# Kernel optimization log

Hardware: AMD Instinct MI355X
Metric: run time of the kernel (lower is better)

Reference implementation:

```python
import jax, jax.numpy as jnp
import numpy as np

EPS = 1e-12
W_MAX = 0.8
ALPHA_MAX = 1.5
EXP_CLIP = 20.0
UNARY_TEMP = 1.5
T = 10
ETA = 0.2
ALPHA_SCALE = 1.0

N_NODES = 50000
N_PAIRS = 400000          # undirected pairs; E = 2*N_PAIRS directed edges
IN_DIM = 256
HID = 128
C = 10
EDGE_HID = 64


def setup_inputs() -> dict:
    key = jax.random.key(0)
    ks = jax.random.split(key, 12)
    x = jax.random.normal(ks[0], (N_NODES, IN_DIM), dtype=jnp.float32)
    # symmetric edge list: each undirected pair appears in both directions,
    # rev[e] gives the index of the reversed edge
    src = jax.random.randint(ks[1], (N_PAIRS,), 0, N_NODES, dtype=jnp.int32)
    dst = jax.random.randint(ks[2], (N_PAIRS,), 0, N_NODES, dtype=jnp.int32)
    edge_index = jnp.stack([jnp.concatenate([src, dst]),
                            jnp.concatenate([dst, src])])  # [2, E]
    rev = jnp.concatenate([jnp.arange(N_PAIRS, 2 * N_PAIRS, dtype=jnp.int32),
                           jnp.arange(0, N_PAIRS, dtype=jnp.int32)])
    def lin(k, fan_in, fan_out):
        s = 1.0 / np.sqrt(fan_in)
        return jax.random.uniform(k, (fan_in, fan_out), jnp.float32, -s, s)
    enc_w1 = lin(ks[3], IN_DIM, HID); enc_b1 = jnp.zeros((HID,), jnp.float32)
    enc_w2 = lin(ks[4], HID, C);      enc_b2 = jnp.zeros((C,), jnp.float32)
    em_in = 2 * HID + 2
    em_w1 = lin(ks[5], em_in, EDGE_HID); em_b1 = jnp.zeros((EDGE_HID,), jnp.float32)
    em_w2 = lin(ks[6], EDGE_HID, 1);     em_b2 = jnp.zeros((1,), jnp.float32)
    # xavier_uniform for R_raw
    bound = np.sqrt(6.0 / (C + C))
    R_raw = jax.random.uniform(ks[7], (C, C), jnp.float32, -bound, bound)
    R_scale_log = jnp.asarray(0.0, jnp.float32)
    msg_logit = jnp.asarray(-1.0, jnp.float32)
    return {"x": x, "edge_index": edge_index, "rev": rev,
            "enc_w1": enc_w1, "enc_b1": enc_b1, "enc_w2": enc_w2, "enc_b2": enc_b2,
            "em_w1": em_w1, "em_b1": em_b1, "em_w2": em_w2, "em_b2": em_b2,
            "R_raw": R_raw, "R_scale_log": R_scale_log, "msg_logit": msg_logit}


def reference(x, edge_index, rev, enc_w1, enc_b1, enc_w2, enc_b2,
              em_w1, em_b1, em_w2, em_b2, R_raw, R_scale_log, msg_logit):
    num_nodes = x.shape[0]
    src, dst = edge_index[0], edge_index[1]

    # --- UnaryEncoder (mlp, eval mode: no dropout) ---
    h = jax.nn.relu(x @ enc_w1 + enc_b1)                       # [N, H]
    logits = h @ enc_w2 + enc_b2                               # [N, C]
    log_phi = jax.nn.log_softmax(logits / UNARY_TEMP, axis=-1)

    # --- edge structural features ---
    deg = jax.ops.segment_sum(jnp.ones_like(src, jnp.float32), src,
                              num_segments=num_nodes)           # bincount(src)
    logdeg = jnp.log(deg + 1.0)
    a, b = logdeg[src], logdeg[dst]
    struct = jnp.stack([a + b, jnp.abs(a - b)], axis=-1)        # [E, 2]

    # --- pairwise kernel ---
    hs, hd = h[src], h[dst]
    edge_in = jnp.concatenate([hs * hd, jnp.abs(hs - hd), struct], axis=-1)
    w_raw = (jax.nn.relu(edge_in @ em_w1 + em_b1) @ em_w2 + em_b2)[:, 0]
    w = W_MAX * jax.nn.sigmoid(w_raw)
    w = 0.5 * (w + w[rev])                                      # symmetrize
    R = (jax.nn.softplus(R_scale_log) + 1e-6) * jnp.tanh(0.5 * (R_raw + R_raw.T))
    K = jnp.exp(jnp.clip(w[:, None, None] * R[None], -EXP_CLIP, EXP_CLIP))  # [E,C,C]

    # --- BP ---
    deg_c = jnp.maximum(deg, 1.0)
    edge_norm = (deg_c[src] * deg_c[dst]) ** -0.5               # [E]
    alpha = ALPHA_MAX * jax.nn.sigmoid(msg_logit) * ALPHA_SCALE
    lp_src = log_phi[src]
    m0 = jax.nn.softmax(lp_src, axis=-1)                        # init_unary=True

    def step(m, _):
        f = jnp.einsum('ec,ecd->ed', m, K)
        f = jnp.nan_to_num(f, nan=1.0, posinf=1.0, neginf=1.0)
        log_f = jnp.log(jnp.maximum(f, EPS)) * edge_norm[:, None]
        sum_in = jax.ops.segment_sum(log_f, dst, num_segments=num_nodes)
        excl = sum_in[src] - log_f[rev]
        m_new = jax.nn.softmax(lp_src + alpha * excl, axis=-1)
        m = (1.0 - ETA) * m + ETA * m_new
        m = jnp.maximum(m, EPS)
        m = m / jnp.sum(m, axis=-1, keepdims=True)
        return m, None

    m, _ = jax.lax.scan(step, m0, None, length=T)

    # --- beliefs ---
    f = jnp.einsum('ec,ecd->ed', m, K)
    f = jnp.nan_to_num(f, nan=1.0, posinf=1.0, neginf=1.0)
    log_f = jnp.log(jnp.maximum(f, EPS)) * edge_norm[:, None]
    sum_in = jax.ops.segment_sum(log_f, dst, num_segments=num_nodes)
    beliefs = jax.nn.softmax(log_phi + alpha * sum_in, axis=-1)  # [N, C]
    return beliefs
```

## Files before the change

kernel.cpp:

```cpp
#include <hip/hip_runtime.h>
#include <hip/hip_fp16.h>

#define NN 50000
#define NP 400000
#define NEDGE 800000
#define IND 256
#define HD 128
#define NC 10
#define TBP 10
#define SCAN_NB 196

typedef _Float16 f16;
typedef _Float16 f16x2 __attribute__((ext_vector_type(2)));
typedef _Float16 f16x4 __attribute__((ext_vector_type(4)));
typedef _Float16 f16x8 __attribute__((ext_vector_type(8)));
typedef unsigned short u16x8 __attribute__((ext_vector_type(8)));
typedef float f32x4 __attribute__((ext_vector_type(4)));

static constexpr size_t OFF_R      = 0;
static constexpr size_t OFF_H      = 512;
static constexpr size_t OFF_OFFS   = 512;
static constexpr size_t OFF_CUR    = 512 + 200016;
static constexpr size_t OFF_CSR    = 512 + 400032;
static constexpr size_t OFF_BSUM   = 512 + 3600032;
static constexpr size_t OFF_BBASE  = 512 + 3601056;
static constexpr size_t OFF_LOGPHI = 12800512;
static constexpr size_t OFF_DEG    = 14800512;
static constexpr size_t OFF_LOGDEG = 15000512;
static constexpr size_t OFF_RSQ    = 15200512;
static constexpr size_t OFF_WPAIR  = 15400512;
static constexpr size_t OFF_EN     = 17000512;
static constexpr size_t OFF_M      = 18600512;
static constexpr size_t OFF_L      = 50600512;
static constexpr size_t OFF_SUMIN  = 82600512;
static constexpr size_t OFF_W1T    = 84600512;
static constexpr size_t OFF_W1TE   = 84633280;

__global__ __launch_bounds__(256) void k_setup(const float* __restrict__ Rraw,
    const float* __restrict__ rsl, const float* __restrict__ ml,
    const float* __restrict__ mw1, const float* __restrict__ ew1,
    float* __restrict__ Rbuf, f16* __restrict__ w1t, f16* __restrict__ w1te) {
  int tid = threadIdx.x;
  if (tid < 100) {
    int c = tid / 10, d = tid % 10;
    float scale = log1pf(expf(rsl[0])) + 1e-6f;
    Rbuf[tid] = scale * tanhf(0.5f * (Rraw[c * 10 + d] + Rraw[d * 10 + c]));
  } else if (tid == 100) {
    Rbuf[100] = 1.5f * (1.f / (1.f + expf(-ml[0])));
  }
  for (int idx = tid; idx < 64 * 256; idx += 256) {
    int j = idx >> 8, k = idx & 255;
    w1t[idx] = (f16)mw1[k * 64 + j];
  }
  for (int idx = tid; idx < 128 * 256; idx += 256) {
    int j = idx >> 8, k = idx & 255;
    w1te[idx] = (f16)ew1[k * HD + j];
  }
}

__global__ __launch_bounds__(256) void k_deg(const int* __restrict__ ei, float* __restrict__ deg) {
  int e = blockIdx.x * 256 + threadIdx.x;
  if (e < NEDGE) atomicAdd(&deg[ei[e]], 1.f);
}

__global__ __launch_bounds__(256) void k_nodepost(const float* __restrict__ deg,
    float* __restrict__ logdeg, float* __restrict__ rsq) {
  int i = blockIdx.x * 256 + threadIdx.x;
  if (i >= NN) return;
  float d = deg[i];
  logdeg[i] = __logf(d + 1.f);
  rsq[i] = rsqrtf(fmaxf(d, 1.f));
}

__global__ __launch_bounds__(256) void k_scan1(const float* __restrict__ deg,
    int* __restrict__ bsum) {
  int idx = blockIdx.x * 256 + threadIdx.x;
  int v = (idx < NN) ? (int)deg[idx] : 0;
#pragma unroll
  for (int o = 32; o; o >>= 1) v += __shfl_down(v, o);
  __shared__ int wsum[4];
  if ((threadIdx.x & 63) == 0) wsum[threadIdx.x >> 6] = v;
  __syncthreads();
  if (threadIdx.x == 0) bsum[blockIdx.x] = wsum[0] + wsum[1] + wsum[2] + wsum[3];
}

__global__ __launch_bounds__(256) void k_scan2(const int* __restrict__ bsum,
    int* __restrict__ bbase) {
  __shared__ int s[256];
  int t = threadIdx.x;
  int orig = (t < SCAN_NB) ? bsum[t] : 0;
  s[t] = orig;
  __syncthreads();
  for (int d = 1; d < 256; d <<= 1) {
    int v = (t >= d) ? s[t - d] : 0;
    __syncthreads();
    s[t] += v;
    __syncthreads();
  }
  bbase[t] = s[t] - orig;
}

__global__ __launch_bounds__(256) void k_scan3(const float* __restrict__ deg,
    const int* __restrict__ bbase, int* __restrict__ off, int* __restrict__ cursor) {
  __shared__ int s[256];
  int t = threadIdx.x;
  int idx = blockIdx.x * 256 + t;
  int d = (idx < NN) ? (int)deg[idx] : 0;
  s[t] = d;
  __syncthreads();
  for (int k = 1; k < 256; k <<= 1) {
    int v = (t >= k) ? s[t - k] : 0;
    __syncthreads();
    s[t] += v;
    __syncthreads();
  }
  int base = bbase[blockIdx.x];
  int excl = base + s[t] - d;
  if (idx < NN) {
    off[idx] = excl;
    cursor[idx] = excl;
  }
  if (idx == NN - 1) off[NN] = excl + d;
}

__global__ __launch_bounds__(256) void k_fill(const int* __restrict__ ei,
    int* __restrict__ cursor, int* __restrict__ csr) {
  int e = blockIdx.x * 256 + threadIdx.x;
  if (e >= NEDGE) return;
  int d = ei[NEDGE + e];
  int pos = atomicAdd(&cursor[d], 1);
  csr[pos] = e;
}

__global__ __launch_bounds__(256) void k_encoder(const float* __restrict__ x,
    const f16* __restrict__ w1te, const float* __restrict__ b1, f16* __restrict__ h) {
  __shared__ f16 As[64 * 264];
  const int tid = threadIdx.x;
  const int wid = tid >> 6;
  const int lane = tid & 63;
  const int l15 = lane & 15;
  const int lhi = lane >> 4;
  const int nb = blockIdx.x * 64;
#pragma unroll
  for (int i = 0; i < 16; i++) {
    int fidx = tid + 256 * i;
    int row = fidx >> 6;
    int q = fidx & 63;
    f32x4 v = {0.f, 0.f, 0.f, 0.f};
    if (nb + row < NN) v = *(const f32x4*)(x + (size_t)(nb + row) * IND + q * 4);
    f16x4 o;
#pragma unroll
    for (int j = 0; j < 4; j++) o[j] = (f16)v[j];
    *(f16x4*)(&As[row * 264 + q * 4]) = o;
  }
  __syncthreads();
  f16x8 bfr[8][2];
#pragma unroll
  for (int ks = 0; ks < 8; ks++)
#pragma unroll
    for (int t = 0; t < 2; t++)
      bfr[ks][t] = *(const f16x8*)(w1te + (size_t)(wid * 32 + t * 16 + l15) * 256 + ks * 32 + lhi * 8);
  float b1v[2] = {b1[wid * 32 + l15], b1[wid * 32 + 16 + l15]};
  f32x4 acc[4][2] = {};
#pragma unroll
  for (int ks = 0; ks < 8; ks++) {
    f16x8 af[4];
#pragma unroll
    for (int rt = 0; rt < 4; rt++)
      af[rt] = *(const f16x8*)(&As[(rt * 16 + l15) * 264 + ks * 32 + lhi * 8]);
#pragma unroll
    for (int rt = 0; rt < 4; rt++)
#pragma unroll
      for (int t = 0; t < 2; t++)
        acc[rt][t] = __builtin_amdgcn_mfma_f32_16x16x32_f16(af[rt], bfr[ks][t], acc[rt][t], 0, 0, 0);
  }
#pragma unroll
  for (int rt = 0; rt < 4; rt++) {
#pragma unroll
    for (int t = 0; t < 2; t++) {
#pragma unroll
      for (int i = 0; i < 4; i++) {
        int row = nb + rt * 16 + lhi * 4 + i;
        if (row < NN)
          h[(size_t)row * HD + wid * 32 + t * 16 + l15] = (f16)fmaxf(acc[rt][t][i] + b1v[t], 0.f);
      }
    }
  }
}

__global__ __launch_bounds__(256) void k_logits(const f16* __restrict__ h,
    const float* __restrict__ w2, const float* __restrict__ b2, float* __restrict__ logphi) {
  __shared__ float hs[16 * HD];
  __shared__ float lg[16 * NC];
  const int tid = threadIdx.x;
  const int nb = blockIdx.x * 16;
  for (int i = tid; i < 16 * HD / 8; i += 256) {
    f16x8 v = *(const f16x8*)(h + (size_t)nb * HD + i * 8);
#pragma unroll
    for (int u = 0; u < 8; u++) hs[i * 8 + u] = (float)v[u];
  }
  __syncthreads();
  if (tid < 160) {
    int n = tid / 10, c = tid % 10;
    float a = b2[c];
    for (int k = 0; k < HD; k++) a += hs[n * HD + k] * w2[k * NC + c];
    lg[n * NC + c] = a * (1.f / 1.5f);
  }
  __syncthreads();
  if (tid < 16) {
    float mx = -1e30f;
#pragma unroll
    for (int c = 0; c < NC; c++) mx = fmaxf(mx, lg[tid * NC + c]);
    float s = 0.f;
#pragma unroll
    for (int c = 0; c < NC; c++) s += __expf(lg[tid * NC + c] - mx);
    float lse = __logf(s) + mx;
#pragma unroll
    for (int c = 0; c < NC; c++)
      logphi[(size_t)(nb + tid) * NC + c] = lg[tid * NC + c] - lse;
  }
}

__global__ __launch_bounds__(256) void k_edge_mlp(const f16* __restrict__ h,
    const int* __restrict__ ei, const float* __restrict__ logdeg, const float* __restrict__ rsq,
    const f16* __restrict__ w1t, const float* __restrict__ mw1, const float* __restrict__ mb1,
    const float* __restrict__ mw2, const float* __restrict__ mb2,
    float* __restrict__ w_pair, float* __restrict__ en_pair) {
  __shared__ f16 At[4][16 * 264];
  __shared__ float hidl[4][16 * 64];
  __shared__ float sfeat[4][2][16];
  const int tid = threadIdx.x;
  const int wid = tid >> 6;
  const int lane = tid & 63;
  const int l15 = lane & 15;
  const int lhi = lane >> 4;

  f16x8 bfr[8][4];
#pragma unroll
  for (int ks = 0; ks < 8; ks++)
#pragma unroll
    for (int t = 0; t < 4; t++)
      bfr[ks][t] = *(const f16x8*)(w1t + (size_t)(l15 + 16 * t) * 256 + ks * 32 + lhi * 8);

  float b1v[4], w256v[4], w257v[4];
#pragma unroll
  for (int t = 0; t < 4; t++) {
    b1v[t] = mb1[l15 + 16 * t];
    w256v[t] = mw1[256 * 64 + l15 + 16 * t];
    w257v[t] = mw1[257 * 64 + l15 + 16 * t];
  }
  float w2r[16];
#pragma unroll
  for (int jj = 0; jj < 16; jj++) w2r[jj] = mw2[lhi * 16 + jj];
  const float b2s = mb2[0];

  const int ntiles = NP / 64;
  for (int tile = blockIdx.x; tile < ntiles; tile += gridDim.x) {
    const int pbase = tile * 64 + wid * 16;
#pragma unroll
    for (int rr = 0; rr < 4; rr++) {
      int r = rr * 4 + lhi;
      int p = pbase + r;
      int s = ei[p], d = ei[NEDGE + p];
      f16x8 hv = *(const f16x8*)(h + (size_t)s * HD + l15 * 8);
      f16x8 gv = *(const f16x8*)(h + (size_t)d * HD + l15 * 8);
      f16x8 pv = hv * gv;
      f16x8 qv = hv - gv;
      u16x8 qb = *(u16x8*)&qv;
#pragma unroll
      for (int u = 0; u < 8; u++) qb[u] &= 0x7FFF;
      qv = *(f16x8*)&qb;
      *(f16x8*)(&At[wid][r * 264 + l15 * 8]) = pv;
      *(f16x8*)(&At[wid][r * 264 + 128 + l15 * 8]) = qv;
    }
    if (lane < 16) {
      int p = pbase + lane;
      int s = ei[p], d = ei[NEDGE + p];
      float a = logdeg[s], b = logdeg[d];
      sfeat[wid][0][lane] = a + b;
      sfeat[wid][1][lane] = fabsf(a - b);
      en_pair[p] = rsq[s] * rsq[d];
    }
    __syncthreads();
    f32x4 acc[4] = {{0.f, 0.f, 0.f, 0.f}, {0.f, 0.f, 0.f, 0.f},
                    {0.f, 0.f, 0.f, 0.f}, {0.f, 0.f, 0.f, 0.f}};
#pragma unroll
    for (int ks = 0; ks < 8; ks++) {
      f16x8 af = *(const f16x8*)(&At[wid][l15 * 264 + ks * 32 + lhi * 8]);
#pragma unroll
      for (int t = 0; t < 4; t++)
        acc[t] = __builtin_amdgcn_mfma_f32_16x16x32_f16(af, bfr[ks][t], acc[t], 0, 0, 0);
    }
#pragma unroll
    for (int t = 0; t < 4; t++) {
#pragma unroll
      for (int i = 0; i < 4; i++) {
        int r = lhi * 4 + i;
        float v = acc[t][i] + sfeat[wid][0][r] * w256v[t] + sfeat[wid][1][r] * w257v[t] + b1v[t];
        hidl[wid][r * 64 + l15 + 16 * t] = fmaxf(v, 0.f);
      }
    }
    __syncthreads();
    {
      float sacc = 0.f;
#pragma unroll
      for (int jj = 0; jj < 16; jj++) sacc += hidl[wid][l15 * 64 + lhi * 16 + jj] * w2r[jj];
      sacc += __shfl_xor(sacc, 16);
      sacc += __shfl_xor(sacc, 32);
      if (lane < 16) {
        float wr = sacc + b2s;
        w_pair[pbase + lane] = 0.8f / (1.f + __expf(-wr));
      }
    }
    __syncthreads();
  }
}

__global__ __launch_bounds__(256) void k_m0(const int* __restrict__ ei,
    const float* __restrict__ logphi, float* __restrict__ m) {
  int e = blockIdx.x * 256 + threadIdx.x;
  if (e >= NEDGE) return;
  int s = ei[e];
  float2* mp = (float2*)(m + (size_t)e * 10);
  const float2* lp = (const float2*)(logphi + (size_t)s * 10);
#pragma unroll
  for (int i = 0; i < 5; i++) {
    float2 v = lp[i];
    float2 o;
    o.x = __expf(v.x);
    o.y = __expf(v.y);
    mp[i] = o;
  }
}

__global__ __launch_bounds__(256) void k_bp_f(const float* __restrict__ m,
    const float* __restrict__ wp, const float* __restrict__ enp,
    const float* __restrict__ Rbuf, f16* __restrict__ L) {
  __shared__ float Rs[100];
  if (threadIdx.x < 100) Rs[threadIdx.x] = Rbuf[threadIdx.x];
  __syncthreads();
  int e = blockIdx.x * 256 + threadIdx.x;
  if (e >= NEDGE) return;
  int p = (e < NP) ? e : e - NP;
  float w = wp[p], en = enp[p];
  float mr[10];
  {
    const float2* mp = (const float2*)(m + (size_t)e * 10);
#pragma unroll
    for (int i = 0; i < 5; i++) { float2 v = mp[i]; mr[2 * i] = v.x; mr[2 * i + 1] = v.y; }
  }
  float f[10] = {0, 0, 0, 0, 0, 0, 0, 0, 0, 0};
#pragma unroll
  for (int c = 0; c < NC; c++) {
    float Ecc = __expf(w * Rs[c * NC + c]);
    f[c] += mr[c] * Ecc;
#pragma unroll
    for (int d = c + 1; d < NC; d++) {
      float Ecd = __expf(w * Rs[c * NC + d]);
      f[d] += mr[c] * Ecd;
      f[c] += mr[d] * Ecd;
    }
  }
  f16x2* Lp = (f16x2*)(L + (size_t)e * 10);
#pragma unroll
  for (int i = 0; i < 5; i++) {
    f16x2 o;
    o[0] = (f16)(__logf(fmaxf(f[2 * i], 1e-12f)) * en);
    o[1] = (f16)(__logf(fmaxf(f[2 * i + 1], 1e-12f)) * en);
    Lp[i] = o;
  }
}

__global__ __launch_bounds__(256) void k_gather(const f16* __restrict__ L,
    const int* __restrict__ csr, const int* __restrict__ off, float* __restrict__ sumin) {
  int wave = (blockIdx.x * 256 + threadIdx.x) >> 6;
  int lane = threadIdx.x & 63;
  int nl = lane / 10;
  int c = lane % 10;
  int n = wave * 6 + nl;
  if (nl >= 6 || n >= NN) return;
  int o0 = off[n], o1 = off[n + 1];
  float acc = 0.f;
  for (int k = o0; k < o1; k++) {
    int e = csr[k];
    acc += (float)L[(size_t)e * 10 + c];
  }
  sumin[(size_t)n * 10 + c] = acc;
}

__global__ __launch_bounds__(256) void k_bp_fused(float* __restrict__ m,
    f16* __restrict__ L, const float* __restrict__ sumin,
    const float* __restrict__ logphi, const int* __restrict__ ei,
    const float* __restrict__ wp, const float* __restrict__ enp,
    const float* __restrict__ Rbuf) {
  __shared__ float Rs[104];
  if (threadIdx.x < 101) Rs[threadIdx.x] = Rbuf[threadIdx.x];
  __syncthreads();
  int p = blockIdx.x * 256 + threadIdx.x;
  if (p >= NP) return;
  const float alpha = Rs[100];
  const int s = ei[p], d = ei[NEDGE + p];
  const float w = wp[p], en = enp[p];

  float Le[10], Lr[10];
  {
    const f16x2* a = (const f16x2*)(L + (size_t)p * 10);
    const f16x2* b = (const f16x2*)(L + (size_t)(p + NP) * 10);
#pragma unroll
    for (int i = 0; i < 5; i++) {
      f16x2 u = a[i], v = b[i];
      Le[2 * i] = (float)u[0]; Le[2 * i + 1] = (float)u[1];
      Lr[2 * i] = (float)v[0]; Lr[2 * i + 1] = (float)v[1];
    }
  }
  float te[10], tr[10];
  float mxe = -1e30f, mxr = -1e30f;
  {
    const float2* sis = (const float2*)(sumin + (size_t)s * 10);
    const float2* sid = (const float2*)(sumin + (size_t)d * 10);
    const float2* lps = (const float2*)(logphi + (size_t)s * 10);
    const float2* lpd = (const float2*)(logphi + (size_t)d * 10);
#pragma unroll
    for (int i = 0; i < 5; i++) {
      float2 ss = sis[i], sd = sid[i], ps = lps[i], pd = lpd[i];
      float e0 = ps.x + alpha * (ss.x - Lr[2 * i]);
      float e1 = ps.y + alpha * (ss.y - Lr[2 * i + 1]);
      float r0 = pd.x + alpha * (sd.x - Le[2 * i]);
      float r1 = pd.y + alpha * (sd.y - Le[2 * i + 1]);
      te[2 * i] = e0; te[2 * i + 1] = e1;
      tr[2 * i] = r0; tr[2 * i + 1] = r1;
      mxe = fmaxf(mxe, fmaxf(e0, e1));
      mxr = fmaxf(mxr, fmaxf(r0, r1));
    }
  }
  float se = 0.f, sr = 0.f;
#pragma unroll
  for (int c = 0; c < NC; c++) {
    float ve = __expf(te[c] - mxe);
    float vr = __expf(tr[c] - mxr);
    te[c] = ve; tr[c] = vr;
    se += ve; sr += vr;
  }
  const float ie = 0.2f / se, ir = 0.2f / sr;
  float me[10], mr[10];
  float nse = 0.f, nsr = 0.f;
  {
    float2* mpe = (float2*)(m + (size_t)p * 10);
    float2* mpr = (float2*)(m + (size_t)(p + NP) * 10);
#pragma unroll
    for (int i = 0; i < 5; i++) {
      float2 u = mpe[i], v = mpr[i];
      float a0 = fmaxf(0.8f * u.x + te[2 * i] * ie, 1e-12f);
      float a1 = fmaxf(0.8f * u.y + te[2 * i + 1] * ie, 1e-12f);
      float b0 = fmaxf(0.8f * v.x + tr[2 * i] * ir, 1e-12f);
      float b1 = fmaxf(0.8f * v.y + tr[2 * i + 1] * ir, 1e-12f);
      me[2 * i] = a0; me[2 * i + 1] = a1;
      mr[2 * i] = b0; mr[2 * i + 1] = b1;
      nse += a0 + a1; nsr += b0 + b1;
    }
    const float qe = 1.f / nse, qr = 1.f / nsr;
#pragma unroll
    for (int i = 0; i < 5; i++) {
      float2 u, v;
      u.x = me[2 * i] * qe; u.y = me[2 * i + 1] * qe;
      v.x = mr[2 * i] * qr; v.y = mr[2 * i + 1] * qr;
      me[2 * i] = u.x; me[2 * i + 1] = u.y;
      mr[2 * i] = v.x; mr[2 * i + 1] = v.y;
      mpe[i] = u; mpr[i] = v;
    }
  }
  float fe[10] = {0, 0, 0, 0, 0, 0, 0, 0, 0, 0};
  float fr[10] = {0, 0, 0, 0, 0, 0, 0, 0, 0, 0};
#pragma unroll
  for (int c = 0; c < NC; c++) {
    float Ecc = __expf(w * Rs[c * NC + c]);
    fe[c] += me[c] * Ecc;
    fr[c] += mr[c] * Ecc;
#pragma unroll
    for (int dd = c + 1; dd < NC; dd++) {
      float E = __expf(w * Rs[c * NC + dd]);
      fe[dd] += me[c] * E; fe[c] += me[dd] * E;
      fr[dd] += mr[c] * E; fr[c] += mr[dd] * E;
    }
  }
  {
    f16x2* Lpe = (f16x2*)(L + (size_t)p * 10);
    f16x2* Lpr = (f16x2*)(L + (size_t)(p + NP) * 10);
#pragma unroll
    for (int i = 0; i < 5; i++) {
      f16x2 u, v;
      u[0] = (f16)(__logf(fmaxf(fe[2 * i], 1e-12f)) * en);
      u[1] = (f16)(__logf(fmaxf(fe[2 * i + 1], 1e-12f)) * en);
      v[0] = (f16)(__logf(fmaxf(fr[2 * i], 1e-12f)) * en);
      v[1] = (f16)(__logf(fmaxf(fr[2 * i + 1], 1e-12f)) * en);
      Lpe[i] = u; Lpr[i] = v;
    }
  }
}

__global__ __launch_bounds__(256) void k_beliefs(const float* __restrict__ logphi,
    const float* __restrict__ sum_in, const float* __restrict__ Rbuf, float* __restrict__ out) {
  int n = blockIdx.x * 256 + threadIdx.x;
  if (n >= NN) return;
  float alpha = Rbuf[100];
  float t[NC];
  float mx = -1e30f;
#pragma unroll
  for (int c = 0; c < NC; c++) {
    float v = logphi[n * NC + c] + alpha * sum_in[n * NC + c];
    t[c] = v;
    mx = fmaxf(mx, v);
  }
  float ssum = 0.f;
#pragma unroll
  for (int c = 0; c < NC; c++) { float ev = __expf(t[c] - mx); t[c] = ev; ssum += ev; }
  float inv = 1.f / ssum;
#pragma unroll
  for (int c = 0; c < NC; c++) out[(size_t)n * NC + c] = t[c] * inv;
}

extern "C" void kernel_launch(void* const* d_in, const int* in_sizes, int n_in,
                              void* d_out, int out_size, void* d_ws, size_t ws_size,
                              hipStream_t stream) {
  const float* x    = (const float*)d_in[0];
  const int*   ei   = (const int*)d_in[1];
  const float* ew1  = (const float*)d_in[3];
  const float* eb1  = (const float*)d_in[4];
  const float* ew2  = (const float*)d_in[5];
  const float* eb2  = (const float*)d_in[6];
  const float* mw1  = (const float*)d_in[7];
  const float* mb1  = (const float*)d_in[8];
  const float* mw2  = (const float*)d_in[9];
  const float* mb2  = (const float*)d_in[10];
  const float* Rraw = (const float*)d_in[11];
  const float* rsl  = (const float*)d_in[12];
  const float* ml   = (const float*)d_in[13];
  float* out = (float*)d_out;

  char* ws = (char*)d_ws;
  float* Rbuf   = (float*)(ws + OFF_R);
  f16*   h      = (f16*)(ws + OFF_H);
  int*   offs   = (int*)(ws + OFF_OFFS);
  int*   cursor = (int*)(ws + OFF_CUR);
  int*   csr    = (int*)(ws + OFF_CSR);
  int*   bsum   = (int*)(ws + OFF_BSUM);
  int*   bbase  = (int*)(ws + OFF_BBASE);
  float* logphi = (float*)(ws + OFF_LOGPHI);
  float* deg    = (float*)(ws + OFF_DEG);
  float* logdeg = (float*)(ws + OFF_LOGDEG);
  float* rsq    = (float*)(ws + OFF_RSQ);
  float* wpair  = (float*)(ws + OFF_WPAIR);
  float* enp    = (float*)(ws + OFF_EN);
  float* m      = (float*)(ws + OFF_M);
  f16*   L      = (f16*)(ws + OFF_L);
  float* sumin  = (float*)(ws + OFF_SUMIN);
  f16*   w1t    = (f16*)(ws + OFF_W1T);
  f16*   w1te   = (f16*)(ws + OFF_W1TE);

  k_setup<<<1, 256, 0, stream>>>(Rraw, rsl, ml, mw1, ew1, Rbuf, w1t, w1te);
  hipMemsetAsync(deg, 0, NN * sizeof(float), stream);
  k_deg<<<NEDGE / 256, 256, 0, stream>>>(ei, deg);
  k_nodepost<<<(NN + 255) / 256, 256, 0, stream>>>(deg, logdeg, rsq);
  k_encoder<<<(NN + 63) / 64, 256, 0, stream>>>(x, w1te, eb1, h);
  k_logits<<<NN / 16, 256, 0, stream>>>(h, ew2, eb2, logphi);
  k_edge_mlp<<<512, 256, 0, stream>>>(h, ei, logdeg, rsq, w1t, mw1, mb1, mw2, mb2, wpair, enp);
  k_scan1<<<SCAN_NB, 256, 0, stream>>>(deg, bsum);
  k_scan2<<<1, 256, 0, stream>>>(bsum, bbase);
  k_scan3<<<SCAN_NB, 256, 0, stream>>>(deg, bbase, offs, cursor);
  k_fill<<<NEDGE / 256, 256, 0, stream>>>(ei, cursor, csr);
  k_m0<<<NEDGE / 256, 256, 0, stream>>>(ei, logphi, m);
  k_bp_f<<<NEDGE / 256, 256, 0, stream>>>(m, wpair, enp, Rbuf, L);

  const int gblocks = (NN + 23) / 24;
  const int fblocks = (NP + 255) / 256;
  for (int it = 0; it < TBP; it++) {
    k_gather<<<gblocks, 256, 0, stream>>>(L, csr, offs, sumin);
    k_bp_fused<<<fblocks, 256, 0, stream>>>(m, L, sumin, logphi, ei, wpair, enp, Rbuf);
  }
  k_gather<<<gblocks, 256, 0, stream>>>(L, csr, offs, sumin);
  k_beliefs<<<(NN + 255) / 256, 256, 0, stream>>>(logphi, sumin, Rbuf, out);
}
```

Measured before the change: 1.084 ms.

## Store log-messages in CSR order and keep messages in fp16

L is now written at each edge's CSR slot (a pos array from k_fill), so the gather kernel reads contiguous rows per node without the csr indirection. The fused BP kernel and the initial f kernel instead do scattered reads and writes of L through pos. Messages m are also stored as fp16 instead of fp32, halving their traffic at some cost in precision.

```diff
diff --git a/kernel.cpp b/kernel.cpp
--- a/kernel.cpp
+++ b/kernel.cpp
@@ -21,7 +21,7 @@
 static constexpr size_t OFF_H      = 512;
 static constexpr size_t OFF_OFFS   = 512;
 static constexpr size_t OFF_CUR    = 512 + 200016;
-static constexpr size_t OFF_CSR    = 512 + 400032;
+static constexpr size_t OFF_POS    = 512 + 400032;
 static constexpr size_t OFF_BSUM   = 512 + 3600032;
 static constexpr size_t OFF_BBASE  = 512 + 3601056;
 static constexpr size_t OFF_LOGPHI = 12800512;
@@ -124,12 +124,11 @@
 }
 
 __global__ __launch_bounds__(256) void k_fill(const int* __restrict__ ei,
-    int* __restrict__ cursor, int* __restrict__ csr) {
+    int* __restrict__ cursor, int* __restrict__ pos) {
   int e = blockIdx.x * 256 + threadIdx.x;
   if (e >= NEDGE) return;
   int d = ei[NEDGE + e];
-  int pos = atomicAdd(&cursor[d], 1);
-  csr[pos] = e;
+  pos[e] = atomicAdd(&cursor[d], 1);
 }
 
 __global__ __launch_bounds__(256) void k_encoder(const float* __restrict__ x,
@@ -317,25 +316,25 @@
 }
 
 __global__ __launch_bounds__(256) void k_m0(const int* __restrict__ ei,
-    const float* __restrict__ logphi, float* __restrict__ m) {
+    const float* __restrict__ logphi, f16* __restrict__ m) {
   int e = blockIdx.x * 256 + threadIdx.x;
   if (e >= NEDGE) return;
   int s = ei[e];
-  float2* mp = (float2*)(m + (size_t)e * 10);
+  f16x2* mp = (f16x2*)(m + (size_t)e * 10);
   const float2* lp = (const float2*)(logphi + (size_t)s * 10);
 #pragma unroll
   for (int i = 0; i < 5; i++) {
     float2 v = lp[i];
-    float2 o;
-    o.x = __expf(v.x);
-    o.y = __expf(v.y);
+    f16x2 o;
+    o[0] = (f16)__expf(v.x);
+    o[1] = (f16)__expf(v.y);
     mp[i] = o;
   }
 }
 
-__global__ __launch_bounds__(256) void k_bp_f(const float* __restrict__ m,
+__global__ __launch_bounds__(256) void k_bp_f(const f16* __restrict__ m,
     const float* __restrict__ wp, const float* __restrict__ enp,
-    const float* __restrict__ Rbuf, f16* __restrict__ L) {
+    const int* __restrict__ pos, const float* __restrict__ Rbuf, f16* __restrict__ L) {
   __shared__ float Rs[100];
   if (threadIdx.x < 100) Rs[threadIdx.x] = Rbuf[threadIdx.x];
   __syncthreads();
@@ -345,9 +344,9 @@
   float w = wp[p], en = enp[p];
   float mr[10];
   {
-    const float2* mp = (const float2*)(m + (size_t)e * 10);
-#pragma unroll
-    for (int i = 0; i < 5; i++) { float2 v = mp[i]; mr[2 * i] = v.x; mr[2 * i + 1] = v.y; }
+    const f16x2* mp = (const f16x2*)(m + (size_t)e * 10);
+#pragma unroll
+    for (int i = 0; i < 5; i++) { f16x2 v = mp[i]; mr[2 * i] = (float)v[0]; mr[2 * i + 1] = (float)v[1]; }
   }
   float f[10] = {0, 0, 0, 0, 0, 0, 0, 0, 0, 0};
 #pragma unroll
@@ -361,7 +360,7 @@
       f[c] += mr[d] * Ecd;
     }
   }
-  f16x2* Lp = (f16x2*)(L + (size_t)e * 10);
+  f16x2* Lp = (f16x2*)(L + (size_t)pos[e] * 10);
 #pragma unroll
   for (int i = 0; i < 5; i++) {
     f16x2 o;
@@ -372,7 +371,7 @@
 }
 
 __global__ __launch_bounds__(256) void k_gather(const f16* __restrict__ L,
-    const int* __restrict__ csr, const int* __restrict__ off, float* __restrict__ sumin) {
+    const int* __restrict__ off, float* __restrict__ sumin) {
   int wave = (blockIdx.x * 256 + threadIdx.x) >> 6;
   int lane = threadIdx.x & 63;
   int nl = lane / 10;
@@ -381,16 +380,14 @@
   if (nl >= 6 || n >= NN) return;
   int o0 = off[n], o1 = off[n + 1];
   float acc = 0.f;
-  for (int k = o0; k < o1; k++) {
-    int e = csr[k];
-    acc += (float)L[(size_t)e * 10 + c];
-  }
+  for (int k = o0; k < o1; k++) acc += (float)L[(size_t)k * 10 + c];
   sumin[(size_t)n * 10 + c] = acc;
 }
 
-__global__ __launch_bounds__(256) void k_bp_fused(float* __restrict__ m,
+__global__ __launch_bounds__(256) void k_bp_fused(f16* __restrict__ m,
     f16* __restrict__ L, const float* __restrict__ sumin,
     const float* __restrict__ logphi, const int* __restrict__ ei,
+    const int* __restrict__ pos,
     const float* __restrict__ wp, const float* __restrict__ enp,
     const float* __restrict__ Rbuf) {
   __shared__ float Rs[104];
@@ -401,11 +398,12 @@
   const float alpha = Rs[100];
   const int s = ei[p], d = ei[NEDGE + p];
   const float w = wp[p], en = enp[p];
+  const int pe = pos[p], pr = pos[p + NP];
 
   float Le[10], Lr[10];
   {
-    const f16x2* a = (const f16x2*)(L + (size_t)p * 10);
-    const f16x2* b = (const f16x2*)(L + (size_t)(p + NP) * 10);
+    const f16x2* a = (const f16x2*)(L + (size_t)pe * 10);
+    const f16x2* b = (const f16x2*)(L + (size_t)pr * 10);
 #pragma unroll
     for (int i = 0; i < 5; i++) {
       f16x2 u = a[i], v = b[i];
@@ -445,15 +443,15 @@
   float me[10], mr[10];
   float nse = 0.f, nsr = 0.f;
   {
-    float2* mpe = (float2*)(m + (size_t)p * 10);
-    float2* mpr = (float2*)(m + (size_t)(p + NP) * 10);
+    f16x2* mpe = (f16x2*)(m + (size_t)p * 10);
+    f16x2* mpr = (f16x2*)(m + (size_t)(p + NP) * 10);
 #pragma unroll
     for (int i = 0; i < 5; i++) {
-      float2 u = mpe[i], v = mpr[i];
-      float a0 = fmaxf(0.8f * u.x + te[2 * i] * ie, 1e-12f);
-      float a1 = fmaxf(0.8f * u.y + te[2 * i + 1] * ie, 1e-12f);
-      float b0 = fmaxf(0.8f * v.x + tr[2 * i] * ir, 1e-12f);
-      float b1 = fmaxf(0.8f * v.y + tr[2 * i + 1] * ir, 1e-12f);
+      f16x2 u = mpe[i], v = mpr[i];
+      float a0 = fmaxf(0.8f * (float)u[0] + te[2 * i] * ie, 1e-12f);
+      float a1 = fmaxf(0.8f * (float)u[1] + te[2 * i + 1] * ie, 1e-12f);
+      float b0 = fmaxf(0.8f * (float)v[0] + tr[2 * i] * ir, 1e-12f);
+      float b1 = fmaxf(0.8f * (float)v[1] + tr[2 * i + 1] * ir, 1e-12f);
       me[2 * i] = a0; me[2 * i + 1] = a1;
       mr[2 * i] = b0; mr[2 * i + 1] = b1;
       nse += a0 + a1; nsr += b0 + b1;
@@ -461,11 +459,11 @@
     const float qe = 1.f / nse, qr = 1.f / nsr;
 #pragma unroll
     for (int i = 0; i < 5; i++) {
-      float2 u, v;
-      u.x = me[2 * i] * qe; u.y = me[2 * i + 1] * qe;
-      v.x = mr[2 * i] * qr; v.y = mr[2 * i + 1] * qr;
-      me[2 * i] = u.x; me[2 * i + 1] = u.y;
-      mr[2 * i] = v.x; mr[2 * i + 1] = v.y;
+      me[2 * i] *= qe; me[2 * i + 1] *= qe;
+      mr[2 * i] *= qr; mr[2 * i + 1] *= qr;
+      f16x2 u, v;
+      u[0] = (f16)me[2 * i]; u[1] = (f16)me[2 * i + 1];
+      v[0] = (f16)mr[2 * i]; v[1] = (f16)mr[2 * i + 1];
       mpe[i] = u; mpr[i] = v;
     }
   }
@@ -484,8 +482,8 @@
     }
   }
   {
-    f16x2* Lpe = (f16x2*)(L + (size_t)p * 10);
-    f16x2* Lpr = (f16x2*)(L + (size_t)(p + NP) * 10);
+    f16x2* Lpe = (f16x2*)(L + (size_t)pe * 10);
+    f16x2* Lpr = (f16x2*)(L + (size_t)pr * 10);
 #pragma unroll
     for (int i = 0; i < 5; i++) {
       f16x2 u, v;
@@ -542,7 +540,7 @@
   f16*   h      = (f16*)(ws + OFF_H);
   int*   offs   = (int*)(ws + OFF_OFFS);
   int*   cursor = (int*)(ws + OFF_CUR);
-  int*   csr    = (int*)(ws + OFF_CSR);
+  int*   pos    = (int*)(ws + OFF_POS);
   int*   bsum   = (int*)(ws + OFF_BSUM);
   int*   bbase  = (int*)(ws + OFF_BBASE);
   float* logphi = (float*)(ws + OFF_LOGPHI);
@@ -551,7 +549,7 @@
   float* rsq    = (float*)(ws + OFF_RSQ);
   float* wpair  = (float*)(ws + OFF_WPAIR);
   float* enp    = (float*)(ws + OFF_EN);
-  float* m      = (float*)(ws + OFF_M);
+  f16*   m      = (f16*)(ws + OFF_M);
   f16*   L      = (f16*)(ws + OFF_L);
   float* sumin  = (float*)(ws + OFF_SUMIN);
   f16*   w1t    = (f16*)(ws + OFF_W1T);
@@ -567,16 +565,16 @@
   k_scan1<<<SCAN_NB, 256, 0, stream>>>(deg, bsum);
   k_scan2<<<1, 256, 0, stream>>>(bsum, bbase);
   k_scan3<<<SCAN_NB, 256, 0, stream>>>(deg, bbase, offs, cursor);
-  k_fill<<<NEDGE / 256, 256, 0, stream>>>(ei, cursor, csr);
+  k_fill<<<NEDGE / 256, 256, 0, stream>>>(ei, cursor, pos);
   k_m0<<<NEDGE / 256, 256, 0, stream>>>(ei, logphi, m);
-  k_bp_f<<<NEDGE / 256, 256, 0, stream>>>(m, wpair, enp, Rbuf, L);
+  k_bp_f<<<NEDGE / 256, 256, 0, stream>>>(m, wpair, enp, pos, Rbuf, L);
 
   const int gblocks = (NN + 23) / 24;
   const int fblocks = (NP + 255) / 256;
   for (int it = 0; it < TBP; it++) {
-    k_gather<<<gblocks, 256, 0, stream>>>(L, csr, offs, sumin);
-    k_bp_fused<<<fblocks, 256, 0, stream>>>(m, L, sumin, logphi, ei, wpair, enp, Rbuf);
-  }
-  k_gather<<<gblocks, 256, 0, stream>>>(L, csr, offs, sumin);
+    k_gather<<<gblocks, 256, 0, stream>>>(L, offs, sumin);
+    k_bp_fused<<<fblocks, 256, 0, stream>>>(m, L, sumin, logphi, ei, pos, wpair, enp, Rbuf);
+  }
+  k_gather<<<gblocks, 256, 0, stream>>>(L, offs, sumin);
   k_beliefs<<<(NN + 255) / 256, 256, 0, stream>>>(logphi, sumin, Rbuf, out);
 }
```

Result: no change. 1.076 ms (-0.7%).
